# Optimization experiments

Hardware: AMD Instinct MI355X
Metric: run time of the kernel (lower is better)

Reference implementation:

```python
import jax, jax.numpy as jnp
import numpy as np

D = 2048; H = 16; DH = D // H; FF = 8192; PFF = 1024
EPS = 1e-6; THETA = 10000.0; CAPACITY = 0.5
BETA_CE = 1.0; BETA_CU = 1.0
SCALE = 0.02

def rms(x, w):
    return x * jax.lax.rsqrt(jnp.mean(x * x, axis=-1, keepdims=True) + EPS) * w

def rope(x, pos):
    # x: [B,H,T,DH], pos: [T]
    inv = 1.0 / (THETA ** (jnp.arange(0, DH, 2, dtype=jnp.float32) / DH))
    ang = pos[:, None] * inv[None, :]                      # [T, DH/2]
    cos = jnp.concatenate([jnp.cos(ang)] * 2, -1)          # [T, DH]
    sin = jnp.concatenate([jnp.sin(ang)] * 2, -1)
    x1, x2 = jnp.split(x, 2, axis=-1)
    rot = jnp.concatenate([-x2, x1], -1)
    return x * cos + rot * sin

def attention(x, wq, wk, wv, wo):
    B, T, _ = x.shape
    pos = jnp.arange(T, dtype=jnp.float32)
    q = (x @ wq).reshape(B, T, H, DH).transpose(0, 2, 1, 3)
    k = (x @ wk).reshape(B, T, H, DH).transpose(0, 2, 1, 3)
    v = (x @ wv).reshape(B, T, H, DH).transpose(0, 2, 1, 3)
    q = rope(q, pos); k = rope(k, pos)
    scores = jnp.einsum('bhqd,bhkd->bhqk', q, k) / np.sqrt(DH).astype(np.float32)
    mask = jnp.tril(jnp.ones((T, T), dtype=bool))
    scores = jnp.where(mask, scores, jnp.finfo(scores.dtype).min)
    probs = jax.nn.softmax(scores, axis=-1)
    out = jnp.einsum('bhqk,bhkd->bhqd', probs, v)
    return out.transpose(0, 2, 1, 3).reshape(B, T, D) @ wo

def swiglu(x, wg, wu, wd):
    return (jax.nn.silu(x @ wg) * (x @ wu)) @ wd

def decoder_layer(x, ln1, ln2, wq, wk, wv, wo, wg, wu, wd):
    h = x + attention(rms(x, ln1), wq, wk, wv, wo)
    return h + swiglu(rms(h, ln2), wg, wu, wd)

def setup_inputs() -> dict:
    key = jax.random.key(0)
    ks = iter(jax.random.split(key, 32))
    def w(shape):
        return SCALE * jax.random.normal(next(ks), shape, dtype=jnp.float32)
    inp = {'hidden_states': jax.random.normal(next(ks), (2, 2048, D), dtype=jnp.float32)}
    for p in ('d1', 'd2'):
        inp[p + '_ln1'] = jnp.ones((D,), jnp.float32)
        inp[p + '_ln2'] = jnp.ones((D,), jnp.float32)
        inp[p + '_wq'] = w((D, D)); inp[p + '_wk'] = w((D, D))
        inp[p + '_wv'] = w((D, D)); inp[p + '_wo'] = w((D, D))
        inp[p + '_wg'] = w((D, FF)); inp[p + '_wu'] = w((D, FF)); inp[p + '_wd'] = w((FF, D))
    inp['p_ln'] = jnp.ones((D,), jnp.float32)
    inp['p_wg'] = w((D, PFF)); inp['p_wu'] = w((D, PFF)); inp['p_wd'] = w((PFF, D))
    return inp

def reference(hidden_states,
              d1_ln1, d1_ln2, d1_wq, d1_wk, d1_wv, d1_wo, d1_wg, d1_wu, d1_wd,
              d2_ln1, d2_ln2, d2_wq, d2_wk, d2_wv, d2_wo, d2_wg, d2_wu, d2_wd,
              p_ln, p_wg, p_wu, p_wd):
    x = hidden_states
    B, T, _ = x.shape
    # decision layer: full decoder block + prior network
    processed = decoder_layer(x, d1_ln1, d1_ln2, d1_wq, d1_wk, d1_wv, d1_wo, d1_wg, d1_wu, d1_wd)
    prior_out = swiglu(rms(x, p_ln), p_wg, p_wu, p_wd)
    prior_hidden = x + prior_out
    actual_res = processed - x                 # [B,T,D]
    pred_res = prior_out                       # prior_hidden - x
    prior_loss = jnp.mean((prior_hidden - jax.lax.stop_gradient(processed)) ** 2)
    # surprise router (VPR-style gate)
    D_st = jnp.mean(actual_res ** 2, axis=-1)                    # [B,T]
    D_ch = jnp.mean((actual_res - pred_res) ** 2, axis=-1)       # [B,T]
    g_cont = jax.nn.sigmoid(BETA_CU * D_ch - BETA_CE * D_st)     # [B,T]
    # top-k token selection per batch row
    k = max(1, int(T * CAPACITY))
    gating_scores, topk_idx = jax.lax.top_k(g_cont, k)           # [B,k]
    # gather -> process through dynamic block -> soft-gate -> scatter
    sel = jnp.take_along_axis(processed, topk_idx[..., None], axis=1)   # [B,k,D]
    sel_out = decoder_layer(sel, d2_ln1, d2_ln2, d2_wq, d2_wk, d2_wv, d2_wo, d2_wg, d2_wu, d2_wd)
    updated = sel + gating_scores[..., None] * (sel_out - sel)   # soft gating (training)
    batch_idx = jnp.arange(B)[:, None]
    final = processed.at[batch_idx, topk_idx].set(updated)
    return final, prior_loss, g_cont
```

## Files before the change

kernel.cpp:

```cpp
#include <hip/hip_runtime.h>
#include <math.h>

#define D_    2048
#define H_    16
#define DH_   128
#define FF_   8192
#define PFF_  1024
#define B_    2
#define T_    2048
#define NTOK_ 4096
#define T2_   1024
#define NSEL_ 2048
#define EPS_  1e-6f
#define SCALE_QK 0.08838834764831845f

typedef __attribute__((ext_vector_type(8))) short bf16x8;
typedef __attribute__((ext_vector_type(4))) float f32x4;
typedef __attribute__((ext_vector_type(8))) unsigned short ushort8;

__device__ __forceinline__ float silu_f(float x) {
    return x / (1.0f + expf(-x));
}

__device__ __forceinline__ unsigned short bf16_rne(float f) {
    unsigned int u = __float_as_uint(f);
    unsigned int r = (u + 0x7fffu + ((u >> 16) & 1u)) >> 16;
    return (unsigned short)r;
}
__device__ __forceinline__ float bf16_tof(unsigned short h) {
    return __uint_as_float(((unsigned int)h) << 16);
}

__global__ __launch_bounds__(256) void rms_kernel(const float* __restrict__ x,
                                                  const float* __restrict__ w,
                                                  float* __restrict__ out) {
    int row = blockIdx.x;
    int tid = threadIdx.x;
    const float4* xr = (const float4*)(x + (size_t)row * D_);
    float4* orow = (float4*)(out + (size_t)row * D_);
    const float4* w4 = (const float4*)w;
    float4 v0 = xr[tid], v1 = xr[tid + 256];
    float s = v0.x*v0.x + v0.y*v0.y + v0.z*v0.z + v0.w*v0.w
            + v1.x*v1.x + v1.y*v1.y + v1.z*v1.z + v1.w*v1.w;
    __shared__ float red[256];
    red[tid] = s; __syncthreads();
    for (int off = 128; off > 0; off >>= 1) {
        if (tid < off) red[tid] += red[tid + off];
        __syncthreads();
    }
    float r = 1.0f / sqrtf(red[0] * (1.0f/2048.0f) + EPS_);
    float4 w0 = w4[tid], w1 = w4[tid + 256];
    float4 o0, o1;
    o0.x = v0.x*r*w0.x; o0.y = v0.y*r*w0.y; o0.z = v0.z*r*w0.z; o0.w = v0.w*r*w0.w;
    o1.x = v1.x*r*w1.x; o1.y = v1.y*r*w1.y; o1.z = v1.z*r*w1.z; o1.w = v1.w*r*w1.w;
    orow[tid] = o0; orow[tid + 256] = o1;
}

template<int WLO>
__global__ __launch_bounds__(256) void splitw_kernel(const float* __restrict__ W,
                                                     unsigned short* __restrict__ phi,
                                                     unsigned short* __restrict__ plo,
                                                     int K, int N) {
    __shared__ float Ts[64][68];
    int n0 = blockIdx.x << 6, k0 = blockIdx.y << 6;
    int tid = threadIdx.x;
#pragma unroll
    for (int it = 0; it < 4; ++it) {
        int idx = tid + (it << 8);
        int kr = idx >> 4, c4 = idx & 15;
        float4 v = *(const float4*)(W + (size_t)(k0 + kr) * N + n0 + (c4 << 2));
        Ts[kr][c4*4+0] = v.x; Ts[kr][c4*4+1] = v.y; Ts[kr][c4*4+2] = v.z; Ts[kr][c4*4+3] = v.w;
    }
    __syncthreads();
#pragma unroll
    for (int h = 0; h < 2; ++h) {
        int c = tid + (h << 8);
        int kc = c >> 6, n = c & 63;
        ushort8 hi, lo;
#pragma unroll
        for (int q = 0; q < 8; ++q) {
            float v = Ts[kc*8 + q][n];
            unsigned short hb = bf16_rne(v);
            hi[q] = hb;
            if (WLO) lo[q] = bf16_rne(v - bf16_tof(hb));
        }
        size_t off = ((size_t)((k0 >> 3) + kc) * N + (n0 + n)) * 8;
        *(ushort8*)(phi + off) = hi;
        if (WLO) *(ushort8*)(plo + off) = lo;
    }
}

template<int WLO>
__global__ __launch_bounds__(256) void splita_kernel(const float* __restrict__ A,
                                                     unsigned short* __restrict__ phi,
                                                     unsigned short* __restrict__ plo,
                                                     int M, int K) {
    __shared__ float Ts[64][68];
    int m0 = blockIdx.x << 6, k0 = blockIdx.y << 6;
    int tid = threadIdx.x;
#pragma unroll
    for (int it = 0; it < 4; ++it) {
        int idx = tid + (it << 8);
        int mr = idx >> 4, c4 = idx & 15;
        float4 v = *(const float4*)(A + (size_t)(m0 + mr) * K + k0 + (c4 << 2));
        Ts[mr][c4*4+0] = v.x; Ts[mr][c4*4+1] = v.y; Ts[mr][c4*4+2] = v.z; Ts[mr][c4*4+3] = v.w;
    }
    __syncthreads();
#pragma unroll
    for (int h = 0; h < 2; ++h) {
        int c = tid + (h << 8);
        int kc = c >> 6, m = c & 63;
        const float* src = &Ts[m][kc << 3];
        ushort8 hi, lo;
#pragma unroll
        for (int q = 0; q < 8; ++q) {
            float v = src[q];
            unsigned short hb = bf16_rne(v);
            hi[q] = hb;
            if (WLO) lo[q] = bf16_rne(v - bf16_tof(hb));
        }
        size_t off = ((size_t)((k0 >> 3) + kc) * M + (m0 + m)) * 8;
        *(ushort8*)(phi + off) = hi;
        if (WLO) *(ushort8*)(plo + off) = lo;
    }
}

__device__ __forceinline__ void stage_panel(unsigned short* lds,
                                            const unsigned short* __restrict__ panel,
                                            int ktile, int R, int brow, int tid) {
#pragma unroll
    for (int h = 0; h < 2; ++h) {
        int c = tid + (h << 8);
        const unsigned short* g = panel + ((size_t)((ktile << 2) + (c >> 7)) * R + (brow + (c & 127))) * 8;
        __builtin_amdgcn_global_load_lds((const __attribute__((address_space(1))) void*)g,
                                         (__attribute__((address_space(3))) void*)(lds + (size_t)c * 8),
                                         16, 0, 0);
    }
}

template<int NP, int EPI>
__global__ __launch_bounds__(256) void gemm_mfma(const unsigned short* __restrict__ pah,
                                                 const unsigned short* __restrict__ pal,
                                                 const unsigned short* __restrict__ pbh,
                                                 const unsigned short* __restrict__ pbl,
                                                 float* __restrict__ C,
                                                 const float* __restrict__ Rg,
                                                 unsigned short* __restrict__ Cph,
                                                 unsigned short* __restrict__ Cpl,
                                                 int M, int N, int K) {
    constexpr int NPAN = (NP == 3) ? 2 : 1;
    __shared__ __align__(16) unsigned short As[2][NPAN][4][128][8];
    __shared__ __align__(16) unsigned short Bs[2][NPAN][4][128][8];
    const int tid = threadIdx.x;
    int nwg = gridDim.x * gridDim.y;
    int wg = blockIdx.y * gridDim.x + blockIdx.x;
    if ((nwg & 7) == 0) {
        int cpx = nwg >> 3;
        wg = (wg & 7) * cpx + (wg >> 3);
    }
    const int bxs = wg / gridDim.y, bys = wg % gridDim.y;
    const int bm = bys << 7, bn = bxs << 7;
    const int lane = tid & 63, wave = tid >> 6;
    const int wm = (wave >> 1) << 6, wn = (wave & 1) << 6;
    const int fr = lane & 15, fk = lane >> 4;

    f32x4 acc[4][4];
#pragma unroll
    for (int i = 0; i < 4; ++i)
#pragma unroll
        for (int j = 0; j < 4; ++j) acc[i][j] = (f32x4)0.0f;

    const int nkt = K >> 5;

    stage_panel(&As[0][0][0][0][0], pah, 0, M, bm, tid);
    if (NP == 3) stage_panel(&As[0][1][0][0][0], pal, 0, M, bm, tid);
    stage_panel(&Bs[0][0][0][0][0], pbh, 0, N, bn, tid);
    if (NP == 3) stage_panel(&Bs[0][1][0][0][0], pbl, 0, N, bn, tid);
    __syncthreads();

    int cur = 0;
    for (int kt = 0; kt < nkt; ++kt) {
        if (kt + 1 < nkt) {
            int nxt = cur ^ 1;
            stage_panel(&As[nxt][0][0][0][0], pah, kt + 1, M, bm, tid);
            if (NP == 3) stage_panel(&As[nxt][1][0][0][0], pal, kt + 1, M, bm, tid);
            stage_panel(&Bs[nxt][0][0][0][0], pbh, kt + 1, N, bn, tid);
            if (NP == 3) stage_panel(&Bs[nxt][1][0][0][0], pbl, kt + 1, N, bn, tid);
        }

        bf16x8 ah[4], bh[4], al[4], bl[4];
#pragma unroll
        for (int i = 0; i < 4; ++i) {
            ah[i] = *(const bf16x8*)&As[cur][0][fk][wm + (i << 4) + fr][0];
            if (NP == 3) al[i] = *(const bf16x8*)&As[cur][NPAN-1][fk][wm + (i << 4) + fr][0];
        }
#pragma unroll
        for (int j = 0; j < 4; ++j) {
            bh[j] = *(const bf16x8*)&Bs[cur][0][fk][wn + (j << 4) + fr][0];
            if (NP == 3) bl[j] = *(const bf16x8*)&Bs[cur][NPAN-1][fk][wn + (j << 4) + fr][0];
        }
#pragma unroll
        for (int i = 0; i < 4; ++i)
#pragma unroll
            for (int j = 0; j < 4; ++j) {
                acc[i][j] = __builtin_amdgcn_mfma_f32_16x16x32_bf16(ah[i], bh[j], acc[i][j], 0, 0, 0);
                if (NP == 3) {
                    acc[i][j] = __builtin_amdgcn_mfma_f32_16x16x32_bf16(ah[i], bl[j], acc[i][j], 0, 0, 0);
                    acc[i][j] = __builtin_amdgcn_mfma_f32_16x16x32_bf16(al[i], bh[j], acc[i][j], 0, 0, 0);
                }
            }
        __syncthreads();
        cur ^= 1;
    }

#pragma unroll
    for (int i = 0; i < 4; ++i) {
        int row0 = bm + wm + (i << 4) + (fk << 2);
#pragma unroll
        for (int j = 0; j < 4; ++j) {
            int col = bn + wn + (j << 4) + fr;
#pragma unroll
            for (int r = 0; r < 4; ++r) {
                int row = row0 + r;
                size_t off = (size_t)row * N + col;
                float v = acc[i][j][r];
                if (EPI == 0) {
                    C[off] = v;
                } else if (EPI == 1) {
                    C[off] = v + Rg[off];
                } else if (EPI == 2) {
                    C[off] = silu_f(Rg[off]) * v;
                } else {
                    v = silu_f(Rg[off]) * v;
                    unsigned short hb = bf16_rne(v);
                    size_t poff = (((size_t)(col >> 3)) * M + row) * 8 + (col & 7);
                    Cph[poff] = hb;
                    if (EPI == 3) Cpl[poff] = bf16_rne(v - bf16_tof(hb));
                }
            }
        }
    }
}

__global__ __launch_bounds__(256) void rope_split_kernel(const float* __restrict__ X,
                                                         unsigned short* __restrict__ xh,
                                                         unsigned short* __restrict__ xl,
                                                         int seqmask, float scale) {
    int tok = blockIdx.x;
    int tid = threadIdx.x;
    int h = tid >> 4, d0 = (tid & 15) << 3;
    int pos = tok & seqmask;
    const float* src = X + (size_t)tok * D_ + h * DH_;
    bool lohalf = d0 < 64;
    float out[8];
#pragma unroll
    for (int q = 0; q < 8; ++q) {
        int d = d0 + q;
        int i = lohalf ? d : (d - 64);
        float e = (float)(2 * i) * (1.0f / 128.0f);
        float inv = 1.0f / powf(10000.0f, e);
        float ang = (float)pos * inv;
        float c = cosf(ang), s = sinf(ang);
        float x1 = src[i], x2 = src[i + 64];
        out[q] = lohalf ? (x1 * c - x2 * s) : (x2 * c + x1 * s);
    }
    ushort8 hi, lo;
#pragma unroll
    for (int q = 0; q < 8; ++q) {
        float v = out[q] * scale;
        unsigned short hb = bf16_rne(v);
        hi[q] = hb;
        lo[q] = bf16_rne(v - bf16_tof(hb));
    }
    size_t off = (size_t)tok * D_ + h * DH_ + d0;
    *(ushort8*)(xh + off) = hi;
    *(ushort8*)(xl + off) = lo;
}

__global__ __launch_bounds__(256) void vpack_kernel(const float* __restrict__ V,
                                                    unsigned short* __restrict__ vth,
                                                    unsigned short* __restrict__ vtl,
                                                    int T) {
    __shared__ float Ts[64][132];
    int kt = blockIdx.x, bh = blockIdx.y;
    int b = bh >> 4, h = bh & 15;
    int tid = threadIdx.x;
#pragma unroll
    for (int it = 0; it < 8; ++it) {
        int idx = tid + (it << 8);
        int r = idx >> 5, c4 = idx & 31;
        float4 v = *(const float4*)(V + ((size_t)(b * T + kt * 64 + r)) * D_ + h * DH_ + (c4 << 2));
        Ts[r][c4*4+0] = v.x; Ts[r][c4*4+1] = v.y; Ts[r][c4*4+2] = v.z; Ts[r][c4*4+3] = v.w;
    }
    __syncthreads();
    size_t obase = ((size_t)bh * (size_t)(T >> 3) + (size_t)kt * 8) * 1024;
#pragma unroll
    for (int it = 0; it < 4; ++it) {
        int c = tid + (it << 8);
        int kc = c >> 7, dh = c & 127;
        ushort8 hi, lo;
#pragma unroll
        for (int q = 0; q < 8; ++q) {
            float v = Ts[kc * 8 + q][dh];
            unsigned short hb = bf16_rne(v);
            hi[q] = hb;
            lo[q] = bf16_rne(v - bf16_tof(hb));
        }
        *(ushort8*)(vth + obase + (size_t)kc * 1024 + dh * 8) = hi;
        *(ushort8*)(vtl + obase + (size_t)kc * 1024 + dh * 8) = lo;
    }
}

__global__ __launch_bounds__(256) void attn_mfma(const unsigned short* __restrict__ QH,
                                                 const unsigned short* __restrict__ QL,
                                                 const unsigned short* __restrict__ KH,
                                                 const unsigned short* __restrict__ KL,
                                                 const unsigned short* __restrict__ VTH,
                                                 const unsigned short* __restrict__ VTL,
                                                 float* __restrict__ O, int T) {
    __shared__ __align__(16) unsigned short KV[16384];
    __shared__ __align__(16) float Ss[4096];
    __shared__ __align__(16) float mrow[64];
    __shared__ __align__(16) float lrow[64];
    __shared__ __align__(16) float crow[64];

    const int tid = threadIdx.x;
    const int qt = blockIdx.x, bh = blockIdx.y;
    const int b = bh >> 4, h = bh & 15;
    const int lane = tid & 63, w = tid >> 6;
    const int fr = lane & 15, fk = lane >> 4;
    const size_t tok0 = (size_t)b * T;

    char* lds_kv = (char*)&KV[0];
    char* lds_sp = (char*)&Ss[0];

    bf16x8 qfh[4], qfl[4];
    {
        const size_t qoff = (tok0 + (size_t)qt * 64 + w * 16 + fr) * D_ + h * DH_ + fk * 8;
#pragma unroll
        for (int ks = 0; ks < 4; ++ks) {
            qfh[ks] = *(const bf16x8*)(QH + qoff + ks * 32);
            qfl[ks] = *(const bf16x8*)(QL + qoff + ks * 32);
        }
    }
    if (tid < 64) { mrow[tid] = -1e30f; lrow[tid] = 0.f; }

    f32x4 acc[8];
#pragma unroll
    for (int nt = 0; nt < 8; ++nt) acc[nt] = (f32x4)0.f;

    const int srow = tid >> 2, sslot = tid & 3;
    const size_t vbase = (size_t)bh * (size_t)(T >> 3) * 1024;

    for (int kt = 0; kt <= qt; ++kt) {
        __syncthreads();
#pragma unroll
        for (int it = 0; it < 4; ++it) {
            int c = tid + (it << 8);
            int t = c >> 4;
            int sp = (c & 15) ^ (t & 7);
            size_t goff = (tok0 + (size_t)kt * 64 + t) * D_ + h * DH_ + sp * 8;
            __builtin_amdgcn_global_load_lds((const __attribute__((address_space(1))) void*)(KH + goff),
                (__attribute__((address_space(3))) void*)(lds_kv + c * 16), 16, 0, 0);
            __builtin_amdgcn_global_load_lds((const __attribute__((address_space(1))) void*)(KL + goff),
                (__attribute__((address_space(3))) void*)(lds_kv + 16384 + c * 16), 16, 0, 0);
        }
        __syncthreads();
        {
            f32x4 s[4];
#pragma unroll
            for (int nt = 0; nt < 4; ++nt) s[nt] = (f32x4)0.f;
#pragma unroll
            for (int ks = 0; ks < 4; ++ks) {
#pragma unroll
                for (int nt = 0; nt < 4; ++nt) {
                    int n = nt * 16 + fr;
                    int offk = (n * 256 + ks * 64 + fk * 16) ^ ((n & 7) << 4);
                    bf16x8 kfh = *(const bf16x8*)(lds_kv + offk);
                    bf16x8 kfl = *(const bf16x8*)(lds_kv + 16384 + offk);
                    s[nt] = __builtin_amdgcn_mfma_f32_16x16x32_bf16(qfh[ks], kfh, s[nt], 0, 0, 0);
                    s[nt] = __builtin_amdgcn_mfma_f32_16x16x32_bf16(qfh[ks], kfl, s[nt], 0, 0, 0);
                    s[nt] = __builtin_amdgcn_mfma_f32_16x16x32_bf16(qfl[ks], kfh, s[nt], 0, 0, 0);
                }
            }
#pragma unroll
            for (int nt = 0; nt < 4; ++nt)
#pragma unroll
                for (int r = 0; r < 4; ++r) {
                    int row = w * 16 + fk * 4 + r;
                    int col = nt * 16 + fr;
                    *(float*)(lds_sp + ((row * 256 + col * 4) ^ ((row & 7) << 4))) = s[nt][r];
                }
        }
        __syncthreads();
#pragma unroll
        for (int it = 0; it < 4; ++it) {
            int c = tid + (it << 8);
            size_t goff = vbase + (size_t)kt * 8192 + (size_t)c * 8;
            __builtin_amdgcn_global_load_lds((const __attribute__((address_space(1))) void*)(VTH + goff),
                (__attribute__((address_space(3))) void*)(lds_kv + c * 16), 16, 0, 0);
            __builtin_amdgcn_global_load_lds((const __attribute__((address_space(1))) void*)(VTL + goff),
                (__attribute__((address_space(3))) void*)(lds_kv + 16384 + c * 16), 16, 0, 0);
        }
        float p[16];
        float newm, psum, cr, oldl;
        {
            float tmax = -1e30f;
            int colbase = sslot * 16;
#pragma unroll
            for (int q4 = 0; q4 < 4; ++q4) {
                f32x4 sv = *(const f32x4*)(lds_sp + ((srow * 256 + sslot * 64 + q4 * 16) ^ ((srow & 7) << 4)));
#pragma unroll
                for (int e = 0; e < 4; ++e) {
                    float v = sv[e];
                    if (kt == qt && (colbase + q4 * 4 + e) > srow) v = -1e30f;
                    p[q4 * 4 + e] = v;
                    tmax = fmaxf(tmax, v);
                }
            }
            tmax = fmaxf(tmax, __shfl_xor(tmax, 1, 64));
            tmax = fmaxf(tmax, __shfl_xor(tmax, 2, 64));
            float oldm = mrow[srow];
            oldl = lrow[srow];
            newm = fmaxf(oldm, tmax);
            psum = 0.f;
#pragma unroll
            for (int e = 0; e < 16; ++e) { p[e] = expf(p[e] - newm); psum += p[e]; }
            psum += __shfl_xor(psum, 1, 64);
            psum += __shfl_xor(psum, 2, 64);
            cr = expf(oldm - newm);
        }
        __syncthreads();
        {
            ushort8 h0, h1, l0, l1;
#pragma unroll
            for (int e = 0; e < 8; ++e) {
                unsigned short hb = bf16_rne(p[e]);
                h0[e] = hb; l0[e] = bf16_rne(p[e] - bf16_tof(hb));
                unsigned short hb2 = bf16_rne(p[8 + e]);
                h1[e] = hb2; l1[e] = bf16_rne(p[8 + e] - bf16_tof(hb2));
            }
            int base = srow * 128 + sslot * 32;
            int swz = (srow & 7) << 4;
            *(ushort8*)(lds_sp + (base ^ swz)) = h0;
            *(ushort8*)(lds_sp + ((base + 16) ^ swz)) = h1;
            *(ushort8*)(lds_sp + 8192 + (base ^ swz)) = l0;
            *(ushort8*)(lds_sp + 8192 + ((base + 16) ^ swz)) = l1;
            if (sslot == 0) { mrow[srow] = newm; lrow[srow] = oldl * cr + psum; crow[srow] = cr; }
        }
        __syncthreads();
        {
            f32x4 crv = *(const f32x4*)&crow[w * 16 + fk * 4];
#pragma unroll
            for (int nt = 0; nt < 8; ++nt)
#pragma unroll
                for (int r = 0; r < 4; ++r) acc[nt][r] *= crv[r];
            int m = w * 16 + fr;
#pragma unroll
            for (int ks = 0; ks < 2; ++ks) {
                int offp = (m * 128 + ks * 64 + fk * 16) ^ ((m & 7) << 4);
                bf16x8 pfh = *(const bf16x8*)(lds_sp + offp);
                bf16x8 pfl = *(const bf16x8*)(lds_sp + 8192 + offp);
#pragma unroll
                for (int nt = 0; nt < 8; ++nt) {
                    int offv = (ks * 4 + fk) * 2048 + (nt * 16 + fr) * 16;
                    bf16x8 vfh = *(const bf16x8*)(lds_kv + offv);
                    bf16x8 vfl = *(const bf16x8*)(lds_kv + 16384 + offv);
                    acc[nt] = __builtin_amdgcn_mfma_f32_16x16x32_bf16(pfh, vfh, acc[nt], 0, 0, 0);
                    acc[nt] = __builtin_amdgcn_mfma_f32_16x16x32_bf16(pfh, vfl, acc[nt], 0, 0, 0);
                    acc[nt] = __builtin_amdgcn_mfma_f32_16x16x32_bf16(pfl, vfh, acc[nt], 0, 0, 0);
                }
            }
        }
    }
    __syncthreads();
    {
        f32x4 lv = *(const f32x4*)&lrow[w * 16 + fk * 4];
        float* orow = O + (tok0 + (size_t)qt * 64 + w * 16 + fk * 4) * D_ + h * DH_;
#pragma unroll
        for (int r = 0; r < 4; ++r) {
            float inv = 1.0f / lv[r];
#pragma unroll
            for (int nt = 0; nt < 8; ++nt)
                orow[(size_t)r * D_ + nt * 16 + fr] = acc[nt][r] * inv;
        }
    }
}

template<int EPI>
__global__ __launch_bounds__(256) void gemm128(const float* __restrict__ A,
                                               const float* __restrict__ Bm,
                                               float* __restrict__ C,
                                               const float* __restrict__ Rg,
                                               int M, int N, int K) {
    __shared__ float Ast[16][132];
    __shared__ float Bs[16][132];
    int bm = blockIdx.y << 7, bn = blockIdx.x << 7;
    int tid = threadIdx.x;
    int ty = tid >> 4, tx = tid & 15;
    float acc[8][8];
#pragma unroll
    for (int i = 0; i < 8; ++i)
#pragma unroll
        for (int j = 0; j < 8; ++j) acc[i][j] = 0.f;

    for (int k0 = 0; k0 < K; k0 += 16) {
#pragma unroll
        for (int it = 0; it < 2; ++it) {
            int idx = tid + (it << 8);
            int ar = idx >> 2, ac = idx & 3;
            float4 av = *(const float4*)(A + (size_t)(bm + ar) * K + k0 + (ac << 2));
            Ast[ac*4+0][ar] = av.x; Ast[ac*4+1][ar] = av.y;
            Ast[ac*4+2][ar] = av.z; Ast[ac*4+3][ar] = av.w;
            int br = idx >> 5, bc = idx & 31;
            float4 bv = *(const float4*)(Bm + (size_t)(k0 + br) * N + bn + (bc << 2));
            *(float4*)&Bs[br][bc << 2] = bv;
        }
        __syncthreads();
#pragma unroll
        for (int kk = 0; kk < 16; ++kk) {
            float a[8], b[8];
            *(float4*)&a[0] = *(const float4*)&Ast[kk][ty*4];
            *(float4*)&a[4] = *(const float4*)&Ast[kk][64 + ty*4];
            *(float4*)&b[0] = *(const float4*)&Bs[kk][tx*4];
            *(float4*)&b[4] = *(const float4*)&Bs[kk][64 + tx*4];
#pragma unroll
            for (int i = 0; i < 8; ++i)
#pragma unroll
                for (int j = 0; j < 8; ++j)
                    acc[i][j] += a[i] * b[j];
        }
        __syncthreads();
    }
#pragma unroll
    for (int i = 0; i < 8; ++i) {
        int row = bm + ((i < 4) ? (ty*4 + i) : (64 + ty*4 + (i - 4)));
#pragma unroll
        for (int half = 0; half < 2; ++half) {
            int col = bn + half*64 + tx*4;
            size_t off = (size_t)row * N + col;
            const float* ap = &acc[i][half*4];
            float4 r;
            if (EPI == 0) {
                r.x = ap[0]; r.y = ap[1]; r.z = ap[2]; r.w = ap[3];
            } else if (EPI == 1) {
                float4 rv = *(const float4*)(Rg + off);
                r.x = ap[0] + rv.x; r.y = ap[1] + rv.y;
                r.z = ap[2] + rv.z; r.w = ap[3] + rv.w;
            } else {
                float4 gv = *(const float4*)(Rg + off);
                r.x = silu_f(gv.x) * ap[0]; r.y = silu_f(gv.y) * ap[1];
                r.z = silu_f(gv.z) * ap[2]; r.w = silu_f(gv.w) * ap[3];
            }
            *(float4*)(C + off) = r;
        }
    }
}

__global__ __launch_bounds__(256) void rope_kernel(float* __restrict__ q, int nrows, int seqlen) {
    int gid = blockIdx.x * 256 + threadIdx.x;
    int tok = gid >> 10;
    if (tok >= nrows) return;
    int rest = gid & 1023;
    int h = rest >> 6, i = rest & 63;
    int pos = tok % seqlen;
    float e = (float)(2 * i) * (1.0f / 128.0f);
    float inv = 1.0f / powf(10000.0f, e);
    float ang = (float)pos * inv;
    float c = cosf(ang), s = sinf(ang);
    size_t base = (size_t)tok * D_ + h * 128 + i;
    float x1 = q[base], x2 = q[base + 64];
    q[base]      = x1 * c - x2 * s;
    q[base + 64] = x2 * c + x1 * s;
}

__global__ __launch_bounds__(256) void attn_kernel(const float* __restrict__ Q,
                                                   const float* __restrict__ K,
                                                   const float* __restrict__ V,
                                                   float* __restrict__ O,
                                                   int T) {
    int qt = blockIdx.x;
    int bh = blockIdx.y;
    int b = bh >> 4, h = bh & 15;
    int tid = threadIdx.x;

    __shared__ float4 Qs[32][32];
    __shared__ float4 KVs[64][32];
    __shared__ float Sst[32][65];
    __shared__ float mrow[32], lrow[32], crow[32];

    const size_t headoff = (size_t)h * DH_;
    const size_t bbase = (size_t)b * T * D_;

#pragma unroll
    for (int i = 0; i < 4; ++i) {
        int idx = tid + i * 256;
        int r = idx >> 5, ch = idx & 31;
        const float4* src = (const float4*)(Q + bbase + (size_t)(qt*32 + r) * D_ + headoff);
        Qs[r][ch ^ ((r >> 2) & 7)] = src[ch];
    }
    if (tid < 32) { mrow[tid] = -1e30f; lrow[tid] = 0.f; }

    int ty16 = tid >> 4, tx16 = tid & 15;
    int r8 = tid >> 3, q8 = tid & 7;
    float o[2][8];
#pragma unroll
    for (int i = 0; i < 2; ++i)
#pragma unroll
        for (int j = 0; j < 8; ++j) o[i][j] = 0.f;

    int ktmax = (qt * 32 + 31) >> 6;
    for (int kt = 0; kt <= ktmax; ++kt) {
        __syncthreads();
#pragma unroll
        for (int i = 0; i < 8; ++i) {
            int idx = tid + i * 256;
            int r = idx >> 5, ch = idx & 31;
            const float4* src = (const float4*)(K + bbase + (size_t)(kt*64 + r) * D_ + headoff);
            KVs[r][ch ^ ((r >> 2) & 7)] = src[ch];
        }
        __syncthreads();
        {
            float s[2][4];
#pragma unroll
            for (int i = 0; i < 2; ++i)
#pragma unroll
                for (int j = 0; j < 4; ++j) s[i][j] = 0.f;
#pragma unroll
            for (int ch = 0; ch < 32; ++ch) {
                float4 qv[2], kv[4];
#pragma unroll
                for (int i = 0; i < 2; ++i) { int r = ty16*2 + i; qv[i] = Qs[r][ch ^ ((r >> 2) & 7)]; }
#pragma unroll
                for (int j = 0; j < 4; ++j) { int c = tx16*4 + j; kv[j] = KVs[c][ch ^ ((c >> 2) & 7)]; }
#pragma unroll
                for (int i = 0; i < 2; ++i)
#pragma unroll
                    for (int j = 0; j < 4; ++j)
                        s[i][j] += qv[i].x*kv[j].x + qv[i].y*kv[j].y + qv[i].z*kv[j].z + qv[i].w*kv[j].w;
            }
#pragma unroll
            for (int i = 0; i < 2; ++i) {
                int grow = qt*32 + ty16*2 + i;
#pragma unroll
                for (int j = 0; j < 4; ++j) {
                    int gcol = kt*64 + tx16*4 + j;
                    float sv = s[i][j] * SCALE_QK;
                    if (gcol > grow) sv = -1e30f;
                    Sst[ty16*2 + i][tx16*4 + j] = sv;
                }
            }
        }
        __syncthreads();
#pragma unroll
        for (int i = 0; i < 8; ++i) {
            int idx = tid + i * 256;
            int r = idx >> 5, ch = idx & 31;
            const float4* src = (const float4*)(V + bbase + (size_t)(kt*64 + r) * D_ + headoff);
            KVs[r][ch ^ ((r >> 2) & 7)] = src[ch];
        }
        {
            float pv[8];
            float tmax = -1e30f;
#pragma unroll
            for (int c = 0; c < 8; ++c) { pv[c] = Sst[r8][q8*8 + c]; tmax = fmaxf(tmax, pv[c]); }
#pragma unroll
            for (int m = 1; m < 8; m <<= 1) tmax = fmaxf(tmax, __shfl_xor(tmax, m, 64));
            float oldm = mrow[r8];
            float newm = fmaxf(oldm, tmax);
            float psum = 0.f;
#pragma unroll
            for (int c = 0; c < 8; ++c) {
                float p = expf(pv[c] - newm);
                Sst[r8][q8*8 + c] = p;
                psum += p;
            }
#pragma unroll
            for (int m = 1; m < 8; m <<= 1) psum += __shfl_xor(psum, m, 64);
            if (q8 == 0) {
                float crv = expf(oldm - newm);
                crow[r8] = crv;
                lrow[r8] = lrow[r8] * crv + psum;
                mrow[r8] = newm;
            }
        }
        __syncthreads();
        {
            float crv[2];
#pragma unroll
            for (int i = 0; i < 2; ++i) {
                crv[i] = crow[ty16*2 + i];
#pragma unroll
                for (int j = 0; j < 8; ++j) o[i][j] *= crv[i];
            }
#pragma unroll
            for (int kc = 0; kc < 64; ++kc) {
                int swz = (kc >> 2) & 7;
                float4 v0 = KVs[kc][tx16 ^ swz];
                float4 v1 = KVs[kc][(16 + tx16) ^ swz];
#pragma unroll
                for (int i = 0; i < 2; ++i) {
                    float p = Sst[ty16*2 + i][kc];
                    o[i][0] += p*v0.x; o[i][1] += p*v0.y; o[i][2] += p*v0.z; o[i][3] += p*v0.w;
                    o[i][4] += p*v1.x; o[i][5] += p*v1.y; o[i][6] += p*v1.z; o[i][7] += p*v1.w;
                }
            }
        }
    }
#pragma unroll
    for (int i = 0; i < 2; ++i) {
        int r = ty16*2 + i;
        float inv = 1.0f / lrow[r];
        float4 a, bb;
        a.x = o[i][0]*inv; a.y = o[i][1]*inv; a.z = o[i][2]*inv; a.w = o[i][3]*inv;
        bb.x = o[i][4]*inv; bb.y = o[i][5]*inv; bb.z = o[i][6]*inv; bb.w = o[i][7]*inv;
        float* dst = O + bbase + (size_t)(qt*32 + r) * D_ + headoff;
        ((float4*)dst)[tx16] = a;
        ((float4*)dst)[16 + tx16] = bb;
    }
}

__global__ __launch_bounds__(256) void router_kernel(const float* __restrict__ x,
                                                     const float* __restrict__ proc,
                                                     const float* __restrict__ prior,
                                                     float* __restrict__ gbuf,
                                                     float* __restrict__ dchbuf,
                                                     float* __restrict__ gout) {
    int row = blockIdx.x, tid = threadIdx.x;
    const float4* x4 = (const float4*)(x + (size_t)row * D_);
    const float4* p4 = (const float4*)(proc + (size_t)row * D_);
    const float4* r4 = (const float4*)(prior + (size_t)row * D_);
    float sst = 0.f, sch = 0.f;
#pragma unroll
    for (int it = 0; it < 2; ++it) {
        int i = tid + it * 256;
        float4 xv = x4[i], pv = p4[i], rv = r4[i];
        float a0 = pv.x - xv.x, a1 = pv.y - xv.y, a2 = pv.z - xv.z, a3 = pv.w - xv.w;
        sst += a0*a0 + a1*a1 + a2*a2 + a3*a3;
        float d0 = a0 - rv.x, d1 = a1 - rv.y, d2 = a2 - rv.z, d3 = a3 - rv.w;
        sch += d0*d0 + d1*d1 + d2*d2 + d3*d3;
    }
    __shared__ float rs[256], rc[256];
    rs[tid] = sst; rc[tid] = sch; __syncthreads();
    for (int off = 128; off > 0; off >>= 1) {
        if (tid < off) { rs[tid] += rs[tid + off]; rc[tid] += rc[tid + off]; }
        __syncthreads();
    }
    if (tid == 0) {
        float Dst = rs[0] * (1.0f/2048.0f);
        float Dch = rc[0] * (1.0f/2048.0f);
        float g = 1.0f / (1.0f + expf(-(Dch - Dst)));
        gbuf[row] = g; dchbuf[row] = Dch; gout[row] = g;
    }
}

__global__ __launch_bounds__(1024) void loss_kernel(const float* __restrict__ dch, float* __restrict__ out) {
    __shared__ float red[1024];
    int tid = threadIdx.x;
    red[tid] = dch[tid] + dch[tid + 1024] + dch[tid + 2048] + dch[tid + 3072];
    __syncthreads();
    for (int off = 512; off > 0; off >>= 1) {
        if (tid < off) red[tid] += red[tid + off];
        __syncthreads();
    }
    if (tid == 0) out[0] = red[0] * (1.0f / 4096.0f);
}

__global__ __launch_bounds__(1024) void topk_kernel(const float* __restrict__ gbuf,
                                                    int* __restrict__ idxout,
                                                    float* __restrict__ gateout) {
    int b = blockIdx.x, tid = threadIdx.x;
    __shared__ float val[2048];
    __shared__ int idx[2048];
    val[tid] = gbuf[b*2048 + tid];           idx[tid] = tid;
    val[tid + 1024] = gbuf[b*2048 + tid + 1024]; idx[tid + 1024] = tid + 1024;
    __syncthreads();
    for (int kk = 2; kk <= 2048; kk <<= 1) {
        for (int j = kk >> 1; j > 0; j >>= 1) {
            for (int i = tid; i < 2048; i += 1024) {
                int ixj = i ^ j;
                if (ixj > i) {
                    bool up = ((i & kk) == 0);
                    float v1 = val[i], v2 = val[ixj];
                    int i1 = idx[i], i2 = idx[ixj];
                    bool sw = up ? ((v2 > v1) || (v2 == v1 && i2 < i1))
                                 : ((v1 > v2) || (v1 == v2 && i1 < i2));
                    if (sw) { val[i] = v2; val[ixj] = v1; idx[i] = i2; idx[ixj] = i1; }
                }
            }
            __syncthreads();
        }
    }
    if (tid < 1024) {
        idxout[b*1024 + tid] = idx[tid];
        gateout[b*1024 + tid] = val[tid];
    }
}

__global__ __launch_bounds__(256) void gather_kernel(const float* __restrict__ proc,
                                                     const int* __restrict__ idx,
                                                     float* __restrict__ sel) {
    int r = blockIdx.x;
    int b = r >> 10, rr = r & 1023;
    int tok = idx[b*1024 + rr];
    const float4* src = (const float4*)(proc + ((size_t)(b*2048 + tok)) * D_);
    float4* dst = (float4*)(sel + (size_t)r * D_);
    dst[threadIdx.x] = src[threadIdx.x];
    dst[threadIdx.x + 256] = src[threadIdx.x + 256];
}

__global__ __launch_bounds__(256) void copy_kernel(const float* __restrict__ src,
                                                   float* __restrict__ dst, int n4) {
    int i = blockIdx.x * 256 + threadIdx.x;
    if (i < n4) ((float4*)dst)[i] = ((const float4*)src)[i];
}

__global__ __launch_bounds__(256) void scatter_kernel(const float* __restrict__ sel,
                                                      const float* __restrict__ selout,
                                                      const int* __restrict__ idx,
                                                      const float* __restrict__ gate,
                                                      float* __restrict__ outp) {
    int r = blockIdx.x;
    int b = r >> 10, rr = r & 1023;
    int tok = idx[b*1024 + rr];
    float g = gate[b*1024 + rr];
    const float4* s4 = (const float4*)(sel + (size_t)r * D_);
    const float4* o4 = (const float4*)(selout + (size_t)r * D_);
    float4* d4 = (float4*)(outp + ((size_t)(b*2048 + tok)) * D_);
#pragma unroll
    for (int it = 0; it < 2; ++it) {
        int i = threadIdx.x + it * 256;
        float4 a = s4[i], o = o4[i];
        float4 w;
        w.x = a.x + g*(o.x - a.x); w.y = a.y + g*(o.y - a.y);
        w.z = a.z + g*(o.z - a.z); w.w = a.w + g*(o.w - a.w);
        d4[i] = w;
    }
}

extern "C" void kernel_launch(void* const* d_in, const int* in_sizes, int n_in,
                              void* d_out, int out_size, void* d_ws, size_t ws_size,
                              hipStream_t stream) {
    const float* X      = (const float*)d_in[0];
    const float* d1_ln1 = (const float*)d_in[1];
    const float* d1_ln2 = (const float*)d_in[2];
    const float* d1_wq  = (const float*)d_in[3];
    const float* d1_wk  = (const float*)d_in[4];
    const float* d1_wv  = (const float*)d_in[5];
    const float* d1_wo  = (const float*)d_in[6];
    const float* d1_wg  = (const float*)d_in[7];
    const float* d1_wu  = (const float*)d_in[8];
    const float* d1_wd  = (const float*)d_in[9];
    const float* d2_ln1 = (const float*)d_in[10];
    const float* d2_ln2 = (const float*)d_in[11];
    const float* d2_wq  = (const float*)d_in[12];
    const float* d2_wk  = (const float*)d_in[13];
    const float* d2_wv  = (const float*)d_in[14];
    const float* d2_wo  = (const float*)d_in[15];
    const float* d2_wg  = (const float*)d_in[16];
    const float* d2_wu  = (const float*)d_in[17];
    const float* d2_wd  = (const float*)d_in[18];
    const float* p_ln   = (const float*)d_in[19];
    const float* p_wg   = (const float*)d_in[20];
    const float* p_wu   = (const float*)d_in[21];
    const float* p_wd   = (const float*)d_in[22];

    float* out = (float*)d_out;
    float* ws  = (float*)d_ws;

    const size_t BIG = (size_t)NTOK_ * D_;
    const size_t MEG = 1024 * 1024;

    const size_t NEED_NEW = (128 * MEG + 16384) * 4;
    const size_t NEED_OLD = ((5*BIG + (size_t)NTOK_*FF_ + 12288) * 4);

    if (ws_size >= NEED_NEW) {
        float* BUF0 = ws;
        float* BUF1 = ws + 8*MEG;
        float* BUF2 = ws + 16*MEG;
        float* BUF3 = ws + 24*MEG;
        float* BUF4 = ws + 32*MEG;
        float* BUFF = ws + 40*MEG;
        unsigned short* PWhi  = (unsigned short*)(ws + 72*MEG);
        unsigned short* PWlo  = (unsigned short*)(ws + 80*MEG);
        unsigned short* PAhi  = (unsigned short*)(ws + 88*MEG);
        unsigned short* PAlo  = (unsigned short*)(ws + 92*MEG);
        unsigned short* PFhi  = (unsigned short*)(ws + 96*MEG);
        unsigned short* PFlo  = (unsigned short*)(ws + 112*MEG);
        unsigned short* U   = (unsigned short*)(ws + 96*MEG);
        const size_t PK = (size_t)NTOK_ * D_;
        unsigned short* QHp = U;
        unsigned short* QLp = U + PK;
        unsigned short* KHp = U + 2*PK;
        unsigned short* KLp = U + 3*PK;
        unsigned short* VTH = U + 4*PK;
        unsigned short* VTL = U + 5*PK;
        float* SM   = ws + 128*MEG;
        float* gbuf = SM;
        float* dch  = SM + 4096;
        float* gate = SM + 8192;
        int*   idxb = (int*)(SM + 10240);

        float* PROC = out;

        rms_kernel<<<NTOK_, 256, 0, stream>>>(X, d1_ln1, BUF0);
        splita_kernel<1><<<dim3(64, 32), 256, 0, stream>>>(BUF0, PAhi, PAlo, NTOK_, D_);
        splitw_kernel<1><<<dim3(32, 32), 256, 0, stream>>>(d1_wq, PWhi, PWlo, D_, D_);
        gemm_mfma<3,0><<<dim3(16, 32), 256, 0, stream>>>(PAhi, PAlo, PWhi, PWlo, BUF1, nullptr, nullptr, nullptr, NTOK_, D_, D_);
        splitw_kernel<1><<<dim3(32, 32), 256, 0, stream>>>(d1_wk, PWhi, PWlo, D_, D_);
        gemm_mfma<3,0><<<dim3(16, 32), 256, 0, stream>>>(PAhi, PAlo, PWhi, PWlo, BUF2, nullptr, nullptr, nullptr, NTOK_, D_, D_);
        splitw_kernel<1><<<dim3(32, 32), 256, 0, stream>>>(d1_wv, PWhi, PWlo, D_, D_);
        gemm_mfma<3,0><<<dim3(16, 32), 256, 0, stream>>>(PAhi, PAlo, PWhi, PWlo, BUF3, nullptr, nullptr, nullptr, NTOK_, D_, D_);
        rope_split_kernel<<<NTOK_, 256, 0, stream>>>(BUF1, QHp, QLp, T_ - 1, SCALE_QK);
        rope_split_kernel<<<NTOK_, 256, 0, stream>>>(BUF2, KHp, KLp, T_ - 1, 1.0f);
        vpack_kernel<<<dim3(T_/64, B_*H_), 256, 0, stream>>>(BUF3, VTH, VTL, T_);
        attn_mfma<<<dim3(T_/64, B_*H_), 256, 0, stream>>>(QHp, QLp, KHp, KLp, VTH, VTL, BUF4, T_);
        splita_kernel<1><<<dim3(64, 32), 256, 0, stream>>>(BUF4, PAhi, PAlo, NTOK_, D_);
        splitw_kernel<1><<<dim3(32, 32), 256, 0, stream>>>(d1_wo, PWhi, PWlo, D_, D_);
        gemm_mfma<3,1><<<dim3(16, 32), 256, 0, stream>>>(PAhi, PAlo, PWhi, PWlo, BUF2, X, nullptr, nullptr, NTOK_, D_, D_);
        rms_kernel<<<NTOK_, 256, 0, stream>>>(BUF2, d1_ln2, BUF0);
        splita_kernel<1><<<dim3(64, 32), 256, 0, stream>>>(BUF0, PAhi, PAlo, NTOK_, D_);
        splitw_kernel<1><<<dim3(128, 32), 256, 0, stream>>>(d1_wg, PWhi, PWlo, D_, FF_);
        gemm_mfma<3,0><<<dim3(64, 32), 256, 0, stream>>>(PAhi, PAlo, PWhi, PWlo, BUFF, nullptr, nullptr, nullptr, NTOK_, FF_, D_);
        splitw_kernel<1><<<dim3(128, 32), 256, 0, stream>>>(d1_wu, PWhi, PWlo, D_, FF_);
        gemm_mfma<3,3><<<dim3(64, 32), 256, 0, stream>>>(PAhi, PAlo, PWhi, PWlo, nullptr, BUFF, PFhi, PFlo, NTOK_, FF_, D_);
        splitw_kernel<1><<<dim3(32, 128), 256, 0, stream>>>(d1_wd, PWhi, PWlo, FF_, D_);
        gemm_mfma<3,1><<<dim3(16, 32), 256, 0, stream>>>(PFhi, PFlo, PWhi, PWlo, PROC, BUF2, nullptr, nullptr, NTOK_, D_, FF_);

        rms_kernel<<<NTOK_, 256, 0, stream>>>(X, p_ln, BUF0);
        splita_kernel<1><<<dim3(64, 32), 256, 0, stream>>>(BUF0, PAhi, PAlo, NTOK_, D_);
        splitw_kernel<1><<<dim3(16, 32), 256, 0, stream>>>(p_wg, PWhi, PWlo, D_, PFF_);
        gemm_mfma<3,0><<<dim3(8, 32), 256, 0, stream>>>(PAhi, PAlo, PWhi, PWlo, BUFF, nullptr, nullptr, nullptr, NTOK_, PFF_, D_);
        splitw_kernel<1><<<dim3(16, 32), 256, 0, stream>>>(p_wu, PWhi, PWlo, D_, PFF_);
        gemm_mfma<3,3><<<dim3(8, 32), 256, 0, stream>>>(PAhi, PAlo, PWhi, PWlo, nullptr, BUFF, PFhi, PFlo, NTOK_, PFF_, D_);
        splitw_kernel<1><<<dim3(32, 16), 256, 0, stream>>>(p_wd, PWhi, PWlo, PFF_, D_);
        gemm_mfma<3,0><<<dim3(16, 32), 256, 0, stream>>>(PFhi, PFlo, PWhi, PWlo, BUF3, nullptr, nullptr, nullptr, NTOK_, D_, PFF_);

        router_kernel<<<NTOK_, 256, 0, stream>>>(X, PROC, BUF3, gbuf, dch, out + 8388609);
        loss_kernel<<<1, 1024, 0, stream>>>(dch, out + 8388608);
        topk_kernel<<<B_, 1024, 0, stream>>>(gbuf, idxb, gate);
        gather_kernel<<<NSEL_, 256, 0, stream>>>(PROC, idxb, BUF4);

        float* V2 = BUF4 + (size_t)NSEL_ * D_;
        rms_kernel<<<NSEL_, 256, 0, stream>>>(BUF4, d2_ln1, BUF0);
        splita_kernel<0><<<dim3(32, 32), 256, 0, stream>>>(BUF0, PAhi, PAlo, NSEL_, D_);
        splitw_kernel<0><<<dim3(32, 32), 256, 0, stream>>>(d2_wq, PWhi, PWlo, D_, D_);
        gemm_mfma<1,0><<<dim3(16, 16), 256, 0, stream>>>(PAhi, PAlo, PWhi, PWlo, BUF2, nullptr, nullptr, nullptr, NSEL_, D_, D_);
        splitw_kernel<0><<<dim3(32, 32), 256, 0, stream>>>(d2_wk, PWhi, PWlo, D_, D_);
        gemm_mfma<1,0><<<dim3(16, 16), 256, 0, stream>>>(PAhi, PAlo, PWhi, PWlo, BUF3, nullptr, nullptr, nullptr, NSEL_, D_, D_);
        splitw_kernel<0><<<dim3(32, 32), 256, 0, stream>>>(d2_wv, PWhi, PWlo, D_, D_);
        gemm_mfma<1,0><<<dim3(16, 16), 256, 0, stream>>>(PAhi, PAlo, PWhi, PWlo, V2, nullptr, nullptr, nullptr, NSEL_, D_, D_);
        rope_split_kernel<<<NSEL_, 256, 0, stream>>>(BUF2, QHp, QLp, T2_ - 1, SCALE_QK);
        rope_split_kernel<<<NSEL_, 256, 0, stream>>>(BUF3, KHp, KLp, T2_ - 1, 1.0f);
        vpack_kernel<<<dim3(T2_/64, B_*H_), 256, 0, stream>>>(V2, VTH, VTL, T2_);
        attn_mfma<<<dim3(T2_/64, B_*H_), 256, 0, stream>>>(QHp, QLp, KHp, KLp, VTH, VTL, BUF0, T2_);
        splita_kernel<0><<<dim3(32, 32), 256, 0, stream>>>(BUF0, PAhi, PAlo, NSEL_, D_);
        splitw_kernel<0><<<dim3(32, 32), 256, 0, stream>>>(d2_wo, PWhi, PWlo, D_, D_);
        gemm_mfma<1,1><<<dim3(16, 16), 256, 0, stream>>>(PAhi, PAlo, PWhi, PWlo, BUF2, BUF4, nullptr, nullptr, NSEL_, D_, D_);
        rms_kernel<<<NSEL_, 256, 0, stream>>>(BUF2, d2_ln2, BUF0);
        splita_kernel<0><<<dim3(32, 32), 256, 0, stream>>>(BUF0, PAhi, PAlo, NSEL_, D_);
        splitw_kernel<0><<<dim3(128, 32), 256, 0, stream>>>(d2_wg, PWhi, PWlo, D_, FF_);
        gemm_mfma<1,0><<<dim3(64, 16), 256, 0, stream>>>(PAhi, PAlo, PWhi, PWlo, BUFF, nullptr, nullptr, nullptr, NSEL_, FF_, D_);
        splitw_kernel<0><<<dim3(128, 32), 256, 0, stream>>>(d2_wu, PWhi, PWlo, D_, FF_);
        gemm_mfma<1,4><<<dim3(64, 16), 256, 0, stream>>>(PAhi, PAlo, PWhi, PWlo, nullptr, BUFF, PFhi, nullptr, NSEL_, FF_, D_);
        splitw_kernel<0><<<dim3(32, 128), 256, 0, stream>>>(d2_wd, PWhi, PWlo, FF_, D_);
        gemm_mfma<1,1><<<dim3(16, 16), 256, 0, stream>>>(PFhi, PFlo, PWhi, PWlo, BUF3, BUF2, nullptr, nullptr, NSEL_, D_, FF_);

        scatter_kernel<<<NSEL_, 256, 0, stream>>>(BUF4, BUF3, idxb, gate, out);
        return;
    }

    if (ws_size < NEED_OLD) return;

    float* BUF0 = ws;
    float* BUF1 = ws + BIG;
    float* BUF2 = ws + 2*BIG;
    float* BUF3 = ws + 3*BIG;
    float* BUF4 = ws + 4*BIG;
    float* BUFF = ws + 5*BIG;
    float* SM   = BUFF + (size_t)NTOK_ * FF_;
    float* gbuf = SM;
    float* dch  = SM + 4096;
    float* gate = SM + 8192;
    int*   idxb = (int*)(SM + 10240);

    rms_kernel<<<NTOK_, 256, 0, stream>>>(X, d1_ln1, BUF0);
    gemm128<0><<<dim3(16, 32), 256, 0, stream>>>(BUF0, d1_wq, BUF1, nullptr, NTOK_, D_, D_);
    gemm128<0><<<dim3(16, 32), 256, 0, stream>>>(BUF0, d1_wk, BUF2, nullptr, NTOK_, D_, D_);
    gemm128<0><<<dim3(16, 32), 256, 0, stream>>>(BUF0, d1_wv, BUF3, nullptr, NTOK_, D_, D_);
    rope_kernel<<<NTOK_*4, 256, 0, stream>>>(BUF1, NTOK_, T_);
    rope_kernel<<<NTOK_*4, 256, 0, stream>>>(BUF2, NTOK_, T_);
    attn_kernel<<<dim3(T_/32, B_*H_), 256, 0, stream>>>(BUF1, BUF2, BUF3, BUF4, T_);
    gemm128<1><<<dim3(16, 32), 256, 0, stream>>>(BUF4, d1_wo, BUF2, X, NTOK_, D_, D_);
    rms_kernel<<<NTOK_, 256, 0, stream>>>(BUF2, d1_ln2, BUF0);
    gemm128<0><<<dim3(64, 32), 256, 0, stream>>>(BUF0, d1_wg, BUFF, nullptr, NTOK_, FF_, D_);
    gemm128<2><<<dim3(64, 32), 256, 0, stream>>>(BUF0, d1_wu, BUFF, BUFF, NTOK_, FF_, D_);
    gemm128<1><<<dim3(16, 32), 256, 0, stream>>>(BUFF, d1_wd, BUF1, BUF2, NTOK_, D_, FF_);

    rms_kernel<<<NTOK_, 256, 0, stream>>>(X, p_ln, BUF0);
    gemm128<0><<<dim3(8, 32), 256, 0, stream>>>(BUF0, p_wg, BUF4, nullptr, NTOK_, PFF_, D_);
    gemm128<2><<<dim3(8, 32), 256, 0, stream>>>(BUF0, p_wu, BUF4, BUF4, NTOK_, PFF_, D_);
    gemm128<0><<<dim3(16, 32), 256, 0, stream>>>(BUF4, p_wd, BUF3, nullptr, NTOK_, D_, PFF_);

    router_kernel<<<NTOK_, 256, 0, stream>>>(X, BUF1, BUF3, gbuf, dch, out + 8388609);
    loss_kernel<<<1, 1024, 0, stream>>>(dch, out + 8388608);
    topk_kernel<<<B_, 1024, 0, stream>>>(gbuf, idxb, gate);
    gather_kernel<<<NSEL_, 256, 0, stream>>>(BUF1, idxb, BUF4);

    float* V2 = BUF4 + (size_t)NSEL_ * D_;
    rms_kernel<<<NSEL_, 256, 0, stream>>>(BUF4, d2_ln1, BUF0);
    gemm128<0><<<dim3(16, 16), 256, 0, stream>>>(BUF0, d2_wq, BUF2, nullptr, NSEL_, D_, D_);
    gemm128<0><<<dim3(16, 16), 256, 0, stream>>>(BUF0, d2_wk, BUF3, nullptr, NSEL_, D_, D_);
    gemm128<0><<<dim3(16, 16), 256, 0, stream>>>(BUF0, d2_wv, V2, nullptr, NSEL_, D_, D_);
    rope_kernel<<<NSEL_*4, 256, 0, stream>>>(BUF2, NSEL_, T2_);
    rope_kernel<<<NSEL_*4, 256, 0, stream>>>(BUF3, NSEL_, T2_);
    attn_kernel<<<dim3(T2_/32, B_*H_), 256, 0, stream>>>(BUF2, BUF3, V2, BUF0, T2_);
    gemm128<1><<<dim3(16, 16), 256, 0, stream>>>(BUF0, d2_wo, BUF2, BUF4, NSEL_, D_, D_);
    rms_kernel<<<NSEL_, 256, 0, stream>>>(BUF2, d2_ln2, BUF0);
    gemm128<0><<<dim3(64, 16), 256, 0, stream>>>(BUF0, d2_wg, BUFF, nullptr, NSEL_, FF_, D_);
    gemm128<2><<<dim3(64, 16), 256, 0, stream>>>(BUF0, d2_wu, BUFF, BUFF, NSEL_, FF_, D_);
    gemm128<1><<<dim3(16, 16), 256, 0, stream>>>(BUFF, d2_wd, BUF3, BUF2, NSEL_, D_, FF_);

    copy_kernel<<<8192, 256, 0, stream>>>(BUF1, out, (int)(BIG / 4));
    scatter_kernel<<<NSEL_, 256, 0, stream>>>(BUF4, BUF3, idxb, gate, out);
}
```

Baseline: 3.080 ms.

## Fuse RMSNorm with bf16 hi/lo panel split and remap GEMM workgroup order

Adds a fused rms_split kernel that normalizes each row and writes the bf16 hi/lo split panels directly. This removes the fp32 intermediate buffer write and reread, and one launch per normalization site. Separately, the GEMM tile mapping now pairs adjacent N-tiles in the workgroup order to improve L2 reuse of the A/B panels. The fused kernel's panel stores are strided by M per thread, which may make its writes less coalesced than the old split kernel's.

Result: no change. 3.077 ms (-0.1%).

```diff
diff --git a/kernel.cpp b/kernel.cpp
--- a/kernel.cpp
+++ b/kernel.cpp
@@ -54,6 +54,42 @@
     o0.x = v0.x*r*w0.x; o0.y = v0.y*r*w0.y; o0.z = v0.z*r*w0.z; o0.w = v0.w*r*w0.w;
     o1.x = v1.x*r*w1.x; o1.y = v1.y*r*w1.y; o1.z = v1.z*r*w1.z; o1.w = v1.w*r*w1.w;
     orow[tid] = o0; orow[tid + 256] = o1;
+}
+
+template<int WLO>
+__global__ __launch_bounds__(256) void rms_split_kernel(const float* __restrict__ x,
+                                                        const float* __restrict__ w,
+                                                        unsigned short* __restrict__ phi,
+                                                        unsigned short* __restrict__ plo,
+                                                        int M) {
+    int row = blockIdx.x;
+    int tid = threadIdx.x;
+    const float4* xr = (const float4*)(x + (size_t)row * D_);
+    const float4* w4 = (const float4*)w;
+    float4 v0 = xr[tid * 2], v1 = xr[tid * 2 + 1];
+    float s = v0.x*v0.x + v0.y*v0.y + v0.z*v0.z + v0.w*v0.w
+            + v1.x*v1.x + v1.y*v1.y + v1.z*v1.z + v1.w*v1.w;
+    __shared__ float red[256];
+    red[tid] = s; __syncthreads();
+    for (int off = 128; off > 0; off >>= 1) {
+        if (tid < off) red[tid] += red[tid + off];
+        __syncthreads();
+    }
+    float r = 1.0f / sqrtf(red[0] * (1.0f/2048.0f) + EPS_);
+    float4 w0 = w4[tid * 2], w1 = w4[tid * 2 + 1];
+    float o[8];
+    o[0] = v0.x*r*w0.x; o[1] = v0.y*r*w0.y; o[2] = v0.z*r*w0.z; o[3] = v0.w*r*w0.w;
+    o[4] = v1.x*r*w1.x; o[5] = v1.y*r*w1.y; o[6] = v1.z*r*w1.z; o[7] = v1.w*r*w1.w;
+    ushort8 hi, lo;
+#pragma unroll
+    for (int q = 0; q < 8; ++q) {
+        unsigned short hb = bf16_rne(o[q]);
+        hi[q] = hb;
+        if (WLO) lo[q] = bf16_rne(o[q] - bf16_tof(hb));
+    }
+    size_t off = ((size_t)tid * M + row) * 8;
+    *(ushort8*)(phi + off) = hi;
+    if (WLO) *(ushort8*)(plo + off) = lo;
 }
 
 template<int WLO>
@@ -158,7 +194,10 @@
         int cpx = nwg >> 3;
         wg = (wg & 7) * cpx + (wg >> 3);
     }
-    const int bxs = wg / gridDim.y, bys = wg % gridDim.y;
+    const int gy2 = gridDim.y << 1;
+    const int sc = wg / gy2;
+    const int wr = wg - sc * gy2;
+    const int bxs = (sc << 1) + (wr & 1), bys = wr >> 1;
     const int bm = bys << 7, bn = bxs << 7;
     const int lane = tid & 63, wave = tid >> 6;
     const int wm = (wave >> 1) << 6, wn = (wave & 1) << 6;
@@ -903,8 +942,7 @@
 
         float* PROC = out;
 
-        rms_kernel<<<NTOK_, 256, 0, stream>>>(X, d1_ln1, BUF0);
-        splita_kernel<1><<<dim3(64, 32), 256, 0, stream>>>(BUF0, PAhi, PAlo, NTOK_, D_);
+        rms_split_kernel<1><<<NTOK_, 256, 0, stream>>>(X, d1_ln1, PAhi, PAlo, NTOK_);
         splitw_kernel<1><<<dim3(32, 32), 256, 0, stream>>>(d1_wq, PWhi, PWlo, D_, D_);
         gemm_mfma<3,0><<<dim3(16, 32), 256, 0, stream>>>(PAhi, PAlo, PWhi, PWlo, BUF1, nullptr, nullptr, nullptr, NTOK_, D_, D_);
         splitw_kernel<1><<<dim3(32, 32), 256, 0, stream>>>(d1_wk, PWhi, PWlo, D_, D_);
@@ -918,8 +956,7 @@
         splita_kernel<1><<<dim3(64, 32), 256, 0, stream>>>(BUF4, PAhi, PAlo, NTOK_, D_);
         splitw_kernel<1><<<dim3(32, 32), 256, 0, stream>>>(d1_wo, PWhi, PWlo, D_, D_);
         gemm_mfma<3,1><<<dim3(16, 32), 256, 0, stream>>>(PAhi, PAlo, PWhi, PWlo, BUF2, X, nullptr, nullptr, NTOK_, D_, D_);
-        rms_kernel<<<NTOK_, 256, 0, stream>>>(BUF2, d1_ln2, BUF0);
-        splita_kernel<1><<<dim3(64, 32), 256, 0, stream>>>(BUF0, PAhi, PAlo, NTOK_, D_);
+        rms_split_kernel<1><<<NTOK_, 256, 0, stream>>>(BUF2, d1_ln2, PAhi, PAlo, NTOK_);
         splitw_kernel<1><<<dim3(128, 32), 256, 0, stream>>>(d1_wg, PWhi, PWlo, D_, FF_);
         gemm_mfma<3,0><<<dim3(64, 32), 256, 0, stream>>>(PAhi, PAlo, PWhi, PWlo, BUFF, nullptr, nullptr, nullptr, NTOK_, FF_, D_);
         splitw_kernel<1><<<dim3(128, 32), 256, 0, stream>>>(d1_wu, PWhi, PWlo, D_, FF_);
@@ -927,8 +964,7 @@
         splitw_kernel<1><<<dim3(32, 128), 256, 0, stream>>>(d1_wd, PWhi, PWlo, FF_, D_);
         gemm_mfma<3,1><<<dim3(16, 32), 256, 0, stream>>>(PFhi, PFlo, PWhi, PWlo, PROC, BUF2, nullptr, nullptr, NTOK_, D_, FF_);
 
-        rms_kernel<<<NTOK_, 256, 0, stream>>>(X, p_ln, BUF0);
-        splita_kernel<1><<<dim3(64, 32), 256, 0, stream>>>(BUF0, PAhi, PAlo, NTOK_, D_);
+        rms_split_kernel<1><<<NTOK_, 256, 0, stream>>>(X, p_ln, PAhi, PAlo, NTOK_);
         splitw_kernel<1><<<dim3(16, 32), 256, 0, stream>>>(p_wg, PWhi, PWlo, D_, PFF_);
         gemm_mfma<3,0><<<dim3(8, 32), 256, 0, stream>>>(PAhi, PAlo, PWhi, PWlo, BUFF, nullptr, nullptr, nullptr, NTOK_, PFF_, D_);
         splitw_kernel<1><<<dim3(16, 32), 256, 0, stream>>>(p_wu, PWhi, PWlo, D_, PFF_);
@@ -942,8 +978,7 @@
         gather_kernel<<<NSEL_, 256, 0, stream>>>(PROC, idxb, BUF4);
 
         float* V2 = BUF4 + (size_t)NSEL_ * D_;
-        rms_kernel<<<NSEL_, 256, 0, stream>>>(BUF4, d2_ln1, BUF0);
-        splita_kernel<0><<<dim3(32, 32), 256, 0, stream>>>(BUF0, PAhi, PAlo, NSEL_, D_);
+        rms_split_kernel<0><<<NSEL_, 256, 0, stream>>>(BUF4, d2_ln1, PAhi, PAlo, NSEL_);
         splitw_kernel<0><<<dim3(32, 32), 256, 0, stream>>>(d2_wq, PWhi, PWlo, D_, D_);
         gemm_mfma<1,0><<<dim3(16, 16), 256, 0, stream>>>(PAhi, PAlo, PWhi, PWlo, BUF2, nullptr, nullptr, nullptr, NSEL_, D_, D_);
         splitw_kernel<0><<<dim3(32, 32), 256, 0, stream>>>(d2_wk, PWhi, PWlo, D_, D_);
@@ -957,8 +992,7 @@
         splita_kernel<0><<<dim3(32, 32), 256, 0, stream>>>(BUF0, PAhi, PAlo, NSEL_, D_);
         splitw_kernel<0><<<dim3(32, 32), 256, 0, stream>>>(d2_wo, PWhi, PWlo, D_, D_);
         gemm_mfma<1,1><<<dim3(16, 16), 256, 0, stream>>>(PAhi, PAlo, PWhi, PWlo, BUF2, BUF4, nullptr, nullptr, NSEL_, D_, D_);
-        rms_kernel<<<NSEL_, 256, 0, stream>>>(BUF2, d2_ln2, BUF0);
-        splita_kernel<0><<<dim3(32, 32), 256, 0, stream>>>(BUF0, PAhi, PAlo, NSEL_, D_);
+        rms_split_kernel<0><<<NSEL_, 256, 0, stream>>>(BUF2, d2_ln2, PAhi, PAlo, NSEL_);
         splitw_kernel<0><<<dim3(128, 32), 256, 0, stream>>>(d2_wg, PWhi, PWlo, D_, FF_);
         gemm_mfma<1,0><<<dim3(64, 16), 256, 0, stream>>>(PAhi, PAlo, PWhi, PWlo, BUFF, nullptr, nullptr, nullptr, NSEL_, FF_, D_);
         splitw_kernel<0><<<dim3(128, 32), 256, 0, stream>>>(d2_wu, PWhi, PWlo, D_, FF_);
```
